# Kernel tuning notes

Measured on AMD Instinct MI355X. Metric: run time of the kernel, lower is better.

The kernel has to match this reference:

```python
import jax, jax.numpy as jnp
import numpy as np

NUM_CLASSES = 256
MARGIN = 0.3
EPS = 1e-12  # torch F.normalize eps


def setup_inputs() -> dict:
    key = jax.random.key(0)
    k1, k2 = jax.random.split(key)
    embeddings = jax.random.normal(k1, (65536, 512), dtype=jnp.float32)
    labels = jax.random.randint(k2, (65536,), 0, NUM_CLASSES)
    return {"embeddings": embeddings, "labels": labels}


def _l2_normalize(x):
    n = jnp.linalg.norm(x, axis=-1, keepdims=True)
    return x / jnp.maximum(n, EPS)


def reference(embeddings, labels):
    # emb_norm: (B, d)
    emb = _l2_normalize(embeddings)

    # Per-class segment mean -> centroids (C, d)
    counts = jax.ops.segment_sum(jnp.ones((emb.shape[0],), emb.dtype), labels,
                                 num_segments=NUM_CLASSES)          # (C,)
    sums = jax.ops.segment_sum(emb, labels, num_segments=NUM_CLASSES)  # (C, d)
    present = counts > 0                                              # (C,)
    cent = sums / jnp.maximum(counts, 1.0)[:, None]
    cent = _l2_normalize(cent)

    # Pairwise centroid euclidean distances (centroids are unit-norm).
    # Only used for argmin (no grad path), so stop_gradient for safety.
    cg = jax.lax.stop_gradient(cent)
    dist = jnp.sqrt(jnp.clip(2.0 - 2.0 * (cg @ cg.T), 0.0))           # (C, C)
    inf = jnp.asarray(jnp.inf, dist.dtype)
    dist = jnp.where(jnp.eye(NUM_CLASSES, dtype=bool), inf, dist)
    dist = jnp.where(present[None, :], dist, inf)  # empty classes can't be negatives
    nearest = jnp.argmin(dist, axis=1)                                # (C,)

    # Gather positive / nearest-negative centroid per sample
    pos_c = cent[labels]                 # (B, d)
    neg_c = cent[nearest[labels]]        # (B, d)
    d_pos = 1.0 - jnp.sum(emb * pos_c, axis=1)
    d_neg = 1.0 - jnp.sum(emb * neg_c, axis=1)
    terms = jax.nn.relu(d_pos - d_neg + MARGIN)                       # (B,)

    # Per-class mean of triplet terms, then mean over present classes
    loss_c = jax.ops.segment_sum(terms, labels, num_segments=NUM_CLASSES)
    loss_c = loss_c / jnp.maximum(counts, 1.0)
    n_present = jnp.maximum(jnp.sum(present.astype(emb.dtype)), 1.0)
    loss = jnp.sum(jnp.where(present, loss_c, 0.0)) / n_present
    return loss
```

## Files before the change

kernel.cpp:

```cpp
#include <hip/hip_runtime.h>
#include <math.h>

#define BROWS 65536
#define DIMS 512
#define NCLS 256
#define MARGIN 0.3f
#define EPSN 1e-12f
#define NSTRIP 64
#define SROWS 1024
#define LSPL 3
#define TSPL 8

__global__ void __launch_bounds__(256) khist2(const int* __restrict__ labels,
                                              int* __restrict__ hist) {
  __shared__ int h[NCLS];
  int t = threadIdx.x, s = blockIdx.x;
  h[t] = 0;
  __syncthreads();
  int base = s * SROWS + t;
#pragma unroll
  for (int k = 0; k < SROWS / 256; ++k) atomicAdd(&h[labels[base + k * 256]], 1);
  __syncthreads();
  hist[s * NCLS + t] = h[t];
}

__global__ void __launch_bounds__(256) kscatter2(const int* __restrict__ labels,
                                                 const int* __restrict__ hist,
                                                 int* __restrict__ bases,
                                                 float* __restrict__ counts,
                                                 int* __restrict__ rowidx) {
  int t = threadIdx.x, s = blockIdx.x;
  int run = 0, myoff = 0;
  for (int s2 = 0; s2 < NSTRIP; ++s2) {
    int h = hist[s2 * NCLS + t];
    if (s2 < s) myoff += h;
    run += h;
  }
  __shared__ int sc[NCLS];
  sc[t] = run;
  __syncthreads();
  int v = sc[t];
  for (int off = 1; off < NCLS; off <<= 1) {
    int add = (t >= off) ? sc[t - off] : 0;
    __syncthreads();
    sc[t] = v = v + add;
    __syncthreads();
  }
  int excl = (t == 0) ? 0 : sc[t - 1];
  if (s == 0) {
    bases[t] = excl;
    counts[t] = (float)run;
  }
  __shared__ int loff[NCLS];
  __shared__ int cur[NCLS];
  loff[t] = excl + myoff;
  cur[t] = 0;
  __syncthreads();
  int rbase = s * SROWS + t;
#pragma unroll
  for (int k = 0; k < SROWS / 256; ++k) {
    int r = rbase + k * 256;
    int lab = labels[r];
    int lpos = atomicAdd(&cur[lab], 1);
    rowidx[loff[lab] + lpos] = r;
  }
}

__global__ void __launch_bounds__(256) ksumn(const float* __restrict__ emb,
                                             const int* __restrict__ rowidx,
                                             const int* __restrict__ bases,
                                             const float* __restrict__ counts,
                                             float* __restrict__ invnorm,
                                             float* __restrict__ partials) {
  int cls = blockIdx.x >> LSPL;
  int sp = blockIdx.x & ((1 << LSPL) - 1);
  int t = threadIdx.x, w = t >> 6, lane = t & 63;
  int base = bases[cls];
  int cnt = (int)counts[cls];
  int i0 = (cnt * sp) >> LSPL;
  int i1 = (cnt * (sp + 1)) >> LSPL;
  int n = i1 - i0;
  int j0 = i0 + ((n * w) >> 2);
  int j1 = i0 + ((n * (w + 1)) >> 2);
  const float4* ebase = reinterpret_cast<const float4*>(emb);
  int cq = lane * 2;
  float4 acc0 = make_float4(0.f, 0.f, 0.f, 0.f);
  float4 acc1 = make_float4(0.f, 0.f, 0.f, 0.f);
  int j = j0;
  for (; j + 4 <= j1; j += 4) {
    int r[4];
#pragma unroll
    for (int k = 0; k < 4; ++k) r[k] = rowidx[base + j + k];
    float4 a[4], b[4];
#pragma unroll
    for (int k = 0; k < 4; ++k) {
      const float4* p = ebase + (size_t)r[k] * (DIMS / 4) + cq;
      a[k] = p[0];
      b[k] = p[1];
    }
    float s[4];
#pragma unroll
    for (int k = 0; k < 4; ++k)
      s[k] = a[k].x*a[k].x + a[k].y*a[k].y + a[k].z*a[k].z + a[k].w*a[k].w
           + b[k].x*b[k].x + b[k].y*b[k].y + b[k].z*b[k].z + b[k].w*b[k].w;
#pragma unroll
    for (int off = 1; off < 64; off <<= 1) {
#pragma unroll
      for (int k = 0; k < 4; ++k) s[k] += __shfl_xor(s[k], off, 64);
    }
    float q[4];
#pragma unroll
    for (int k = 0; k < 4; ++k) q[k] = 1.0f / fmaxf(sqrtf(s[k]), EPSN);
    if (lane == 0) {
      invnorm[r[0]] = q[0]; invnorm[r[1]] = q[1];
      invnorm[r[2]] = q[2]; invnorm[r[3]] = q[3];
    }
#pragma unroll
    for (int k = 0; k < 4; ++k) {
      acc0.x += a[k].x * q[k]; acc0.y += a[k].y * q[k];
      acc0.z += a[k].z * q[k]; acc0.w += a[k].w * q[k];
      acc1.x += b[k].x * q[k]; acc1.y += b[k].y * q[k];
      acc1.z += b[k].z * q[k]; acc1.w += b[k].w * q[k];
    }
  }
  for (; j < j1; ++j) {
    int r0 = rowidx[base + j];
    const float4* p = ebase + (size_t)r0 * (DIMS / 4) + cq;
    float4 a = p[0], b = p[1];
    float s = a.x*a.x + a.y*a.y + a.z*a.z + a.w*a.w
            + b.x*b.x + b.y*b.y + b.z*b.z + b.w*b.w;
#pragma unroll
    for (int off = 1; off < 64; off <<= 1) s += __shfl_xor(s, off, 64);
    float q0 = 1.0f / fmaxf(sqrtf(s), EPSN);
    if (lane == 0) invnorm[r0] = q0;
    acc0.x += a.x * q0; acc0.y += a.y * q0; acc0.z += a.z * q0; acc0.w += a.w * q0;
    acc1.x += b.x * q0; acc1.y += b.y * q0; acc1.z += b.z * q0; acc1.w += b.w * q0;
  }
  __shared__ float lds[4][DIMS];
  *reinterpret_cast<float4*>(&lds[w][lane * 8]) = acc0;
  *reinterpret_cast<float4*>(&lds[w][lane * 8 + 4]) = acc1;
  __syncthreads();
  float o0 = lds[0][t] + lds[1][t] + lds[2][t] + lds[3][t];
  float o1 = lds[0][t + 256] + lds[1][t + 256] + lds[2][t + 256] + lds[3][t + 256];
  float* outp = partials + ((size_t)sp * NCLS + cls) * DIMS;
  outp[t] = o0;
  outp[t + 256] = o1;
}

__global__ void __launch_bounds__(256) kcent(const float* __restrict__ partials,
                                             const float* __restrict__ counts,
                                             float* __restrict__ cent) {
  int cls = blockIdx.x, t = threadIdx.x;
  float s0 = 0.0f, s1 = 0.0f;
#pragma unroll
  for (int sp = 0; sp < (1 << LSPL); ++sp) {
    const float* p = partials + ((size_t)sp * NCLS + cls) * DIMS;
    s0 += p[t];
    s1 += p[t + 256];
  }
  float cm = fmaxf(counts[cls], 1.0f);
  float m0 = s0 / cm, m1 = s1 / cm;
  __shared__ float red[256];
  red[t] = m0 * m0 + m1 * m1;
  __syncthreads();
  for (int off = 128; off > 0; off >>= 1) {
    if (t < off) red[t] += red[t + off];
    __syncthreads();
  }
  float inv = 1.0f / fmaxf(sqrtf(red[0]), EPSN);
  cent[(size_t)cls * DIMS + t] = m0 * inv;
  cent[(size_t)cls * DIMS + t + 256] = m1 * inv;
}

__global__ void __launch_bounds__(256) knearest(const float* __restrict__ cent,
                                                const float* __restrict__ counts,
                                                int* __restrict__ nearest) {
  int i = blockIdx.x, j = threadIdx.x;
  __shared__ float ci[DIMS];
  ci[j] = cent[(size_t)i * DIMS + j];
  ci[j + 256] = cent[(size_t)i * DIMS + j + 256];
  __syncthreads();
  const float4* cj = reinterpret_cast<const float4*>(cent + (size_t)j * DIMS);
  float dot = 0.0f;
#pragma unroll 8
  for (int k = 0; k < DIMS / 4; ++k) {
    float4 v = cj[k];
    dot += v.x * ci[4*k] + v.y * ci[4*k+1] + v.z * ci[4*k+2] + v.w * ci[4*k+3];
  }
  float dist = sqrtf(fmaxf(2.0f - 2.0f * dot, 0.0f));
  bool valid = (j != i) && (counts[j] > 0.0f);
  float dv = valid ? dist : INFINITY;
  __shared__ float sd[256];
  __shared__ int si[256];
  sd[j] = dv; si[j] = j;
  __syncthreads();
  for (int off = 128; off > 0; off >>= 1) {
    if (j < off) {
      float o = sd[j + off]; int oi = si[j + off];
      if (o < sd[j] || (o == sd[j] && oi < si[j])) { sd[j] = o; si[j] = oi; }
    }
    __syncthreads();
  }
  if (j == 0) nearest[i] = si[0];
}

__global__ void __launch_bounds__(256) kterm2(const float* __restrict__ emb,
                                              const float* __restrict__ invnorm,
                                              const int* __restrict__ rowidx,
                                              const int* __restrict__ bases,
                                              const float* __restrict__ counts,
                                              const float* __restrict__ cent,
                                              const int* __restrict__ nearest,
                                              float* __restrict__ tsums) {
  int cls = blockIdx.x >> 3;
  int sp = blockIdx.x & (TSPL - 1);
  int t = threadIdx.x, w = t >> 6, lane = t & 63;
  int base = bases[cls];
  int cnt = (int)counts[cls];
  int ng = nearest[cls];
  int cq = lane * 2;
  const float4* pp = reinterpret_cast<const float4*>(cent + (size_t)cls * DIMS) + cq;
  const float4* pn = reinterpret_cast<const float4*>(cent + (size_t)ng * DIMS) + cq;
  float4 P0 = pp[0], P1 = pp[1], N0 = pn[0], N1 = pn[1];
  float4 d0 = make_float4(N0.x - P0.x, N0.y - P0.y, N0.z - P0.z, N0.w - P0.w);
  float4 d1 = make_float4(N1.x - P1.x, N1.y - P1.y, N1.z - P1.z, N1.w - P1.w);
  int i0 = (cnt * sp) / TSPL;
  int i1 = (cnt * (sp + 1)) / TSPL;
  int n = i1 - i0;
  int j0 = i0 + ((n * w) >> 2);
  int j1 = i0 + ((n * (w + 1)) >> 2);
  const float4* ebase = reinterpret_cast<const float4*>(emb);
  float tsum = 0.0f;
  int j = j0;
  for (; j + 4 <= j1; j += 4) {
    int r[4];
#pragma unroll
    for (int k = 0; k < 4; ++k) r[k] = rowidx[base + j + k];
    float inv[4];
#pragma unroll
    for (int k = 0; k < 4; ++k) inv[k] = invnorm[r[k]];
    float4 a[4], b[4];
#pragma unroll
    for (int k = 0; k < 4; ++k) {
      const float4* p = ebase + (size_t)r[k] * (DIMS / 4) + cq;
      a[k] = p[0];
      b[k] = p[1];
    }
    float s[4];
#pragma unroll
    for (int k = 0; k < 4; ++k)
      s[k] = a[k].x*d0.x + a[k].y*d0.y + a[k].z*d0.z + a[k].w*d0.w
           + b[k].x*d1.x + b[k].y*d1.y + b[k].z*d1.z + b[k].w*d1.w;
#pragma unroll
    for (int off = 1; off < 64; off <<= 1) {
#pragma unroll
      for (int k = 0; k < 4; ++k) s[k] += __shfl_xor(s[k], off, 64);
    }
#pragma unroll
    for (int k = 0; k < 4; ++k) tsum += fmaxf(s[k] * inv[k] + MARGIN, 0.0f);
  }
  for (; j < j1; ++j) {
    int r0 = rowidx[base + j];
    float inv0 = invnorm[r0];
    const float4* p = ebase + (size_t)r0 * (DIMS / 4) + cq;
    float4 a = p[0], b = p[1];
    float s = a.x*d0.x + a.y*d0.y + a.z*d0.z + a.w*d0.w
            + b.x*d1.x + b.y*d1.y + b.z*d1.z + b.w*d1.w;
#pragma unroll
    for (int off = 1; off < 64; off <<= 1) s += __shfl_xor(s, off, 64);
    tsum += fmaxf(s * inv0 + MARGIN, 0.0f);
  }
  __shared__ float sred[4];
  if (lane == 0) sred[w] = tsum;
  __syncthreads();
  if (t == 0) tsums[blockIdx.x] = sred[0] + sred[1] + sred[2] + sred[3];
}

__global__ void __launch_bounds__(256) kfinal(const float* __restrict__ counts,
                                              const float* __restrict__ tsums,
                                              float* __restrict__ out) {
  int t = threadIdx.x;
  float cnt = counts[t];
  bool present = cnt > 0.0f;
  float ls = 0.0f;
#pragma unroll
  for (int k = 0; k < TSPL; ++k) ls += tsums[t * TSPL + k];
  float v = present ? ls / fmaxf(cnt, 1.0f) : 0.0f;
  float np = present ? 1.0f : 0.0f;
  __shared__ float sv[256], sp[256];
  sv[t] = v; sp[t] = np;
  __syncthreads();
  for (int off = 128; off > 0; off >>= 1) {
    if (t < off) { sv[t] += sv[t + off]; sp[t] += sp[t + off]; }
    __syncthreads();
  }
  if (t == 0) out[0] = sv[0] / fmaxf(sp[0], 1.0f);
}

extern "C" void kernel_launch(void* const* d_in, const int* in_sizes, int n_in,
                              void* d_out, int out_size, void* d_ws, size_t ws_size,
                              hipStream_t stream) {
  const float* emb = (const float*)d_in[0];
  const int* labels = (const int*)d_in[1];
  float* out = (float*)d_out;

  char* ws = (char*)d_ws;
  size_t off = 0;
  auto alloc = [&](size_t bytes) {
    char* p = ws + off;
    off += (bytes + 255) & ~(size_t)255;
    return p;
  };
  int*   hist    = (int*)alloc((size_t)NSTRIP * NCLS * 4);
  int*   bases   = (int*)alloc((size_t)NCLS * 4);
  float* counts  = (float*)alloc((size_t)NCLS * 4);
  float* cent    = (float*)alloc((size_t)NCLS * DIMS * 4);
  int*   nearest = (int*)alloc((size_t)NCLS * 4);
  int*   rowidx  = (int*)alloc((size_t)BROWS * 4);
  float* invnorm = (float*)alloc((size_t)BROWS * 4);
  float* tsums   = (float*)alloc((size_t)NCLS * TSPL * 4);
  float* partials= (float*)alloc(((size_t)NCLS * DIMS * 4) << LSPL);

  khist2<<<NSTRIP, 256, 0, stream>>>(labels, hist);
  kscatter2<<<NSTRIP, 256, 0, stream>>>(labels, hist, bases, counts, rowidx);
  ksumn<<<NCLS << LSPL, 256, 0, stream>>>(emb, rowidx, bases, counts, invnorm, partials);
  kcent<<<NCLS, 256, 0, stream>>>(partials, counts, cent);
  knearest<<<NCLS, 256, 0, stream>>>(cent, counts, nearest);
  kterm2<<<NCLS * TSPL, 256, 0, stream>>>(emb, invnorm, rowidx, bases, counts,
                                          cent, nearest, tsums);
  kfinal<<<1, 256, 0, stream>>>(counts, tsums, out);
}
```

Baseline: 248.3 us.

## Merge launches using grid barrier and last-block-done reductions

Fuses the histogram and scatter kernels with a spin-wait grid barrier over 64 blocks. Centroid normalization now runs in the last-arriving split block of each class, and the final loss reduction runs in the last block of the term kernel, both chosen through atomic counters. This removes three kernel launches and their inter-kernel gaps. In exchange it adds a memset launch, atomic and fence overhead, and relies on all 64 blocks being co-resident for the spin barrier.

```diff
diff --git a/kernel.cpp b/kernel.cpp
--- a/kernel.cpp
+++ b/kernel.cpp
@@ -11,30 +11,33 @@
 #define LSPL 3
 #define TSPL 8
 
-__global__ void __launch_bounds__(256) khist2(const int* __restrict__ labels,
-                                              int* __restrict__ hist) {
-  __shared__ int h[NCLS];
-  int t = threadIdx.x, s = blockIdx.x;
-  h[t] = 0;
-  __syncthreads();
-  int base = s * SROWS + t;
-#pragma unroll
-  for (int k = 0; k < SROWS / 256; ++k) atomicAdd(&h[labels[base + k * 256]], 1);
-  __syncthreads();
-  hist[s * NCLS + t] = h[t];
-}
-
-__global__ void __launch_bounds__(256) kscatter2(const int* __restrict__ labels,
-                                                 const int* __restrict__ hist,
+__global__ void __launch_bounds__(256) kscatter3(const int* __restrict__ labels,
+                                                 int* __restrict__ hist,
+                                                 int* __restrict__ done,
                                                  int* __restrict__ bases,
                                                  float* __restrict__ counts,
                                                  int* __restrict__ rowidx) {
   int t = threadIdx.x, s = blockIdx.x;
+  __shared__ int h[NCLS];
+  h[t] = 0;
+  __syncthreads();
+  int rbase = s * SROWS + t;
+#pragma unroll
+  for (int k = 0; k < SROWS / 256; ++k) atomicAdd(&h[labels[rbase + k * 256]], 1);
+  __syncthreads();
+  hist[s * NCLS + t] = h[t];
+  __threadfence();
+  if (t == 0) {
+    atomicAdd(done, 1);
+    while (atomicAdd(done, 0) < NSTRIP) { }
+  }
+  __syncthreads();
+  __threadfence();
   int run = 0, myoff = 0;
   for (int s2 = 0; s2 < NSTRIP; ++s2) {
-    int h = hist[s2 * NCLS + t];
-    if (s2 < s) myoff += h;
-    run += h;
+    int hv = hist[s2 * NCLS + t];
+    if (s2 < s) myoff += hv;
+    run += hv;
   }
   __shared__ int sc[NCLS];
   sc[t] = run;
@@ -56,7 +59,6 @@
   loff[t] = excl + myoff;
   cur[t] = 0;
   __syncthreads();
-  int rbase = s * SROWS + t;
 #pragma unroll
   for (int k = 0; k < SROWS / 256; ++k) {
     int r = rbase + k * 256;
@@ -66,12 +68,14 @@
   }
 }
 
-__global__ void __launch_bounds__(256) ksumn(const float* __restrict__ emb,
-                                             const int* __restrict__ rowidx,
-                                             const int* __restrict__ bases,
-                                             const float* __restrict__ counts,
-                                             float* __restrict__ invnorm,
-                                             float* __restrict__ partials) {
+__global__ void __launch_bounds__(256) ksumn2(const float* __restrict__ emb,
+                                              const int* __restrict__ rowidx,
+                                              const int* __restrict__ bases,
+                                              const float* __restrict__ counts,
+                                              float* __restrict__ invnorm,
+                                              float* __restrict__ partials,
+                                              int* __restrict__ ccnt,
+                                              float* __restrict__ cent) {
   int cls = blockIdx.x >> LSPL;
   int sp = blockIdx.x & ((1 << LSPL) - 1);
   int t = threadIdx.x, w = t >> 6, lane = t & 63;
@@ -145,31 +149,32 @@
   float* outp = partials + ((size_t)sp * NCLS + cls) * DIMS;
   outp[t] = o0;
   outp[t + 256] = o1;
-}
-
-__global__ void __launch_bounds__(256) kcent(const float* __restrict__ partials,
-                                             const float* __restrict__ counts,
-                                             float* __restrict__ cent) {
-  int cls = blockIdx.x, t = threadIdx.x;
-  float s0 = 0.0f, s1 = 0.0f;
-#pragma unroll
-  for (int sp = 0; sp < (1 << LSPL); ++sp) {
-    const float* p = partials + ((size_t)sp * NCLS + cls) * DIMS;
-    s0 += p[t];
-    s1 += p[t + 256];
-  }
-  float cm = fmaxf(counts[cls], 1.0f);
-  float m0 = s0 / cm, m1 = s1 / cm;
-  __shared__ float red[256];
-  red[t] = m0 * m0 + m1 * m1;
-  __syncthreads();
-  for (int off = 128; off > 0; off >>= 1) {
-    if (t < off) red[t] += red[t + off];
-    __syncthreads();
-  }
-  float inv = 1.0f / fmaxf(sqrtf(red[0]), EPSN);
-  cent[(size_t)cls * DIMS + t] = m0 * inv;
-  cent[(size_t)cls * DIMS + t + 256] = m1 * inv;
+  __threadfence();
+  __shared__ int lastflag;
+  if (t == 0) lastflag = (atomicAdd(&ccnt[cls], 1) == (1 << LSPL) - 1) ? 1 : 0;
+  __syncthreads();
+  if (lastflag) {
+    __threadfence();
+    float s0 = 0.0f, s1 = 0.0f;
+#pragma unroll
+    for (int spp = 0; spp < (1 << LSPL); ++spp) {
+      const float* p = partials + ((size_t)spp * NCLS + cls) * DIMS;
+      s0 += p[t];
+      s1 += p[t + 256];
+    }
+    float cm = fmaxf(counts[cls], 1.0f);
+    float m0 = s0 / cm, m1 = s1 / cm;
+    __shared__ float red[256];
+    red[t] = m0 * m0 + m1 * m1;
+    __syncthreads();
+    for (int off = 128; off > 0; off >>= 1) {
+      if (t < off) red[t] += red[t + off];
+      __syncthreads();
+    }
+    float inv = 1.0f / fmaxf(sqrtf(red[0]), EPSN);
+    cent[(size_t)cls * DIMS + t] = m0 * inv;
+    cent[(size_t)cls * DIMS + t + 256] = m1 * inv;
+  }
 }
 
 __global__ void __launch_bounds__(256) knearest(const float* __restrict__ cent,
@@ -204,14 +209,16 @@
   if (j == 0) nearest[i] = si[0];
 }
 
-__global__ void __launch_bounds__(256) kterm2(const float* __restrict__ emb,
+__global__ void __launch_bounds__(256) kterm3(const float* __restrict__ emb,
                                               const float* __restrict__ invnorm,
                                               const int* __restrict__ rowidx,
                                               const int* __restrict__ bases,
                                               const float* __restrict__ counts,
                                               const float* __restrict__ cent,
                                               const int* __restrict__ nearest,
-                                              float* __restrict__ tsums) {
+                                              float* __restrict__ tsums,
+                                              int* __restrict__ tcnt,
+                                              float* __restrict__ out) {
   int cls = blockIdx.x >> 3;
   int sp = blockIdx.x & (TSPL - 1);
   int t = threadIdx.x, w = t >> 6, lane = t & 63;
@@ -274,27 +281,28 @@
   if (lane == 0) sred[w] = tsum;
   __syncthreads();
   if (t == 0) tsums[blockIdx.x] = sred[0] + sred[1] + sred[2] + sred[3];
-}
-
-__global__ void __launch_bounds__(256) kfinal(const float* __restrict__ counts,
-                                              const float* __restrict__ tsums,
-                                              float* __restrict__ out) {
-  int t = threadIdx.x;
-  float cnt = counts[t];
-  bool present = cnt > 0.0f;
-  float ls = 0.0f;
-#pragma unroll
-  for (int k = 0; k < TSPL; ++k) ls += tsums[t * TSPL + k];
-  float v = present ? ls / fmaxf(cnt, 1.0f) : 0.0f;
-  float np = present ? 1.0f : 0.0f;
-  __shared__ float sv[256], sp[256];
-  sv[t] = v; sp[t] = np;
-  __syncthreads();
-  for (int off = 128; off > 0; off >>= 1) {
-    if (t < off) { sv[t] += sv[t + off]; sp[t] += sp[t + off]; }
-    __syncthreads();
-  }
-  if (t == 0) out[0] = sv[0] / fmaxf(sp[0], 1.0f);
+  __threadfence();
+  __shared__ int lastf;
+  if (t == 0) lastf = (atomicAdd(tcnt, 1) == NCLS * TSPL - 1) ? 1 : 0;
+  __syncthreads();
+  if (lastf) {
+    __threadfence();
+    float cntc = counts[t];
+    bool present = cntc > 0.0f;
+    float ls = 0.0f;
+#pragma unroll
+    for (int k = 0; k < TSPL; ++k) ls += tsums[t * TSPL + k];
+    float v = present ? ls / fmaxf(cntc, 1.0f) : 0.0f;
+    float np = present ? 1.0f : 0.0f;
+    __shared__ float sv[256], spv[256];
+    sv[t] = v; spv[t] = np;
+    __syncthreads();
+    for (int off = 128; off > 0; off >>= 1) {
+      if (t < off) { sv[t] += sv[t + off]; spv[t] += spv[t + off]; }
+      __syncthreads();
+    }
+    if (t == 0) out[0] = sv[0] / fmaxf(spv[0], 1.0f);
+  }
 }
 
 extern "C" void kernel_launch(void* const* d_in, const int* in_sizes, int n_in,
@@ -311,22 +319,25 @@
     off += (bytes + 255) & ~(size_t)255;
     return p;
   };
+  int*   done    = (int*)alloc((size_t)(2 + NCLS) * 4);
+  int*   tcnt    = done + 1;
+  int*   ccnt    = done + 2;
   int*   hist    = (int*)alloc((size_t)NSTRIP * NCLS * 4);
   int*   bases   = (int*)alloc((size_t)NCLS * 4);
   float* counts  = (float*)alloc((size_t)NCLS * 4);
-  float* cent    = (float*)alloc((size_t)NCLS * DIMS * 4);
   int*   nearest = (int*)alloc((size_t)NCLS * 4);
   int*   rowidx  = (int*)alloc((size_t)BROWS * 4);
   float* invnorm = (float*)alloc((size_t)BROWS * 4);
   float* tsums   = (float*)alloc((size_t)NCLS * TSPL * 4);
+  float* cent    = (float*)alloc((size_t)NCLS * DIMS * 4);
   float* partials= (float*)alloc(((size_t)NCLS * DIMS * 4) << LSPL);
 
-  khist2<<<NSTRIP, 256, 0, stream>>>(labels, hist);
-  kscatter2<<<NSTRIP, 256, 0, stream>>>(labels, hist, bases, counts, rowidx);
-  ksumn<<<NCLS << LSPL, 256, 0, stream>>>(emb, rowidx, bases, counts, invnorm, partials);
-  kcent<<<NCLS, 256, 0, stream>>>(partials, counts, cent);
+  hipMemsetAsync(done, 0, (size_t)(2 + NCLS) * 4, stream);
+
+  kscatter3<<<NSTRIP, 256, 0, stream>>>(labels, hist, done, bases, counts, rowidx);
+  ksumn2<<<NCLS << LSPL, 256, 0, stream>>>(emb, rowidx, bases, counts, invnorm,
+                                           partials, ccnt, cent);
   knearest<<<NCLS, 256, 0, stream>>>(cent, counts, nearest);
-  kterm2<<<NCLS * TSPL, 256, 0, stream>>>(emb, invnorm, rowidx, bases, counts,
-                                          cent, nearest, tsums);
-  kfinal<<<1, 256, 0, stream>>>(counts, tsums, out);
-}
+  kterm3<<<NCLS * TSPL, 256, 0, stream>>>(emb, invnorm, rowidx, bases, counts,
+                                          cent, nearest, tsums, tcnt, out);
+}
```

Result: slower. 902.6 us (+263.5%).
